# Kernel optimization log

Measured on AMD Instinct MI355X. Metric: run time of the kernel, lower is better.

The kernel has to match this reference:

```python
import jax, jax.numpy as jnp
import numpy as np

LATENT = 256

def setup_inputs() -> dict:
    key = jax.random.key(0)
    k1, k2, k3, k4, k5 = jax.random.split(key, 5)
    B, Te, Td, D = 4, 512, 256, LATENT
    encoder_output = jax.random.normal(k1, (B, Te, D), dtype=jnp.float32)
    decoder_output = jax.random.normal(k2, (B, Td, D), dtype=jnp.float32)
    # 'random_normal' keras initializer: stddev 0.05
    W_a = jax.random.normal(k3, (D, D), dtype=jnp.float32) * 0.05
    U_a = jax.random.normal(k4, (D, D), dtype=jnp.float32) * 0.05
    V_a = jax.random.normal(k5, (D, 1), dtype=jnp.float32) * 0.05
    return {"encoder_output": encoder_output, "decoder_output": decoder_output,
            "W_a": W_a, "U_a": U_a, "V_a": V_a}

def reference(encoder_output, decoder_output, W_a, U_a, V_a):
    # Projections computed once per position (mathematically equal to the
    # tiled tensordots in the original, without redundant GEMM work).
    W_enc = jnp.einsum('bed,df->bef', encoder_output, W_a)   # [B,Te,D]
    U_dec = jnp.einsum('btd,df->btf', decoder_output, U_a)   # [B,Td,D]
    # Broadcast add replaces the explicit tf.tile: [B,Td,Te,D]
    e = jnp.tanh(W_enc[:, None, :, :] + U_dec[:, :, None, :])
    score = jnp.einsum('bted,do->bte', e, V_a[:, 0:1])        # [B,Td,Te]
    attention_weights = jax.nn.softmax(score, axis=-1)
    context_vector = jnp.einsum('bte,bed->btd', attention_weights, encoder_output)
    return (context_vector, attention_weights)
```

## Files before the change

### kernel.cpp

```cpp
#include <hip/hip_runtime.h>

#define B 4
#define TE 512
#define TD 256
#define D 256

#define C2    2.8853900817779268f
#define LOG2E 1.4426950408889634f

__global__ __launch_bounds__(512) void proj_kernel(
    const float* __restrict__ enc, const float* __restrict__ dec,
    const float* __restrict__ Wa,  const float* __restrict__ Ua,
    float* __restrict__ ewt, float* __restrict__ eu)
{
    __shared__ float a_lds[8 * 256];
    const int tid = threadIdx.x;
    const int blk = blockIdx.x;
    const bool is_enc = blk < 256;
    const float* __restrict__ A = is_enc ? enc : dec;
    const float* __restrict__ W = is_enc ? Wa  : Ua;
    const int row0 = (is_enc ? blk : blk - 256) * 8;

    ((float4*)a_lds)[tid] = ((const float4*)(A + (size_t)row0 * 256))[tid];
    __syncthreads();

    const int rh  = tid >> 8;
    const int col = tid & 255;

    float c0 = 0.f, c1 = 0.f, c2 = 0.f, c3 = 0.f;
    const float* __restrict__ ar = &a_lds[rh * 4 * 256];

    #pragma unroll 4
    for (int k = 0; k < 256; k += 4) {
        const float w0 = W[(k + 0) * 256 + col];
        const float w1 = W[(k + 1) * 256 + col];
        const float w2 = W[(k + 2) * 256 + col];
        const float w3 = W[(k + 3) * 256 + col];
        const float4 a0 = *(const float4*)&ar[0 * 256 + k];
        const float4 a1 = *(const float4*)&ar[1 * 256 + k];
        const float4 a2 = *(const float4*)&ar[2 * 256 + k];
        const float4 a3 = *(const float4*)&ar[3 * 256 + k];
        c0 = fmaf(a0.x, w0, c0); c0 = fmaf(a0.y, w1, c0); c0 = fmaf(a0.z, w2, c0); c0 = fmaf(a0.w, w3, c0);
        c1 = fmaf(a1.x, w0, c1); c1 = fmaf(a1.y, w1, c1); c1 = fmaf(a1.z, w2, c1); c1 = fmaf(a1.w, w3, c1);
        c2 = fmaf(a2.x, w0, c2); c2 = fmaf(a2.y, w1, c2); c2 = fmaf(a2.z, w2, c2); c2 = fmaf(a2.w, w3, c2);
        c3 = fmaf(a3.x, w0, c3); c3 = fmaf(a3.y, w1, c3); c3 = fmaf(a3.z, w2, c3); c3 = fmaf(a3.w, w3, c3);
    }

    float4 f;
    f.x = __builtin_amdgcn_exp2f(c0 * C2);
    f.y = __builtin_amdgcn_exp2f(c1 * C2);
    f.z = __builtin_amdgcn_exp2f(c2 * C2);
    f.w = __builtin_amdgcn_exp2f(c3 * C2);

    if (is_enc) {
        const int b  = row0 >> 9;
        const int e0 = (row0 & 511) + rh * 4;
        *(float4*)&ewt[((size_t)(b * 256 + col)) * 512 + e0] = f;
    } else {
        const int r0 = row0 + rh * 4;
        eu[(r0 + 0) * 256 + col] = f.x;
        eu[(r0 + 1) * 256 + col] = f.y;
        eu[(r0 + 2) * 256 + col] = f.z;
        eu[(r0 + 3) * 256 + col] = f.w;
    }
}

__global__ __launch_bounds__(512) void attn_kernel(
    const float* __restrict__ enc, const float* __restrict__ ewt,
    const float* __restrict__ eu,  const float* __restrict__ Va,
    float* __restrict__ ctx, float* __restrict__ aw)
{
    __shared__ float eul[2 * 256];
    __shared__ float val[256];
    __shared__ float sc[2][TE];
    __shared__ float wred[2][2][4];
    __shared__ float part[2][2][256];

    const int tid = threadIdx.x;
    const int b   = blockIdx.x >> 7;
    const int tp  = blockIdx.x & 127;
    const int bt0 = b * 256 + tp * 2;

    if (tid < 256) val[tid] = Va[tid];
    eul[tid] = eu[(size_t)bt0 * 256 + tid];
    __syncthreads();

    {
        const float* __restrict__ ewb = ewt + (size_t)b * 256 * 512 + tid;
        float q0 = 0.f, q1 = 0.f;

        for (int d = 0; d < 256; d += 8) {
            float w[8];
            #pragma unroll
            for (int j = 0; j < 8; j++) w[j] = ewb[(d + j) * 512];

            #pragma unroll
            for (int h = 0; h < 2; h++) {
                const int dd = d + h * 4;
                const float4 v4 = *(const float4*)&val[dd];
                const float4 a0 = *(const float4*)&eul[dd];
                const float4 a1 = *(const float4*)&eul[256 + dd];
                const float* wj = &w[h * 4];

                q0 += v4.x * __builtin_amdgcn_rcpf(fmaf(wj[0], a0.x, 1.0f));
                q0 += v4.y * __builtin_amdgcn_rcpf(fmaf(wj[1], a0.y, 1.0f));
                q0 += v4.z * __builtin_amdgcn_rcpf(fmaf(wj[2], a0.z, 1.0f));
                q0 += v4.w * __builtin_amdgcn_rcpf(fmaf(wj[3], a0.w, 1.0f));

                q1 += v4.x * __builtin_amdgcn_rcpf(fmaf(wj[0], a1.x, 1.0f));
                q1 += v4.y * __builtin_amdgcn_rcpf(fmaf(wj[1], a1.y, 1.0f));
                q1 += v4.z * __builtin_amdgcn_rcpf(fmaf(wj[2], a1.z, 1.0f));
                q1 += v4.w * __builtin_amdgcn_rcpf(fmaf(wj[3], a1.w, 1.0f));
            }
        }
        sc[0][tid] = -2.0f * q0;
        sc[1][tid] = -2.0f * q1;
    }
    __syncthreads();

    {
        const int wv   = tid >> 6;
        const int lane = tid & 63;
        const int t    = wv >> 2;
        const int seg  = wv & 3;
        float* __restrict__ srow = &sc[t][seg * 128];

        const float x0 = srow[lane];
        const float x1 = srow[lane + 64];

        float m = fmaxf(x0, x1);
        #pragma unroll
        for (int s = 32; s > 0; s >>= 1) m = fmaxf(m, __shfl_xor(m, s, 64));
        if (lane == 0) wred[0][t][seg] = m;
        __syncthreads();
        const float4 mm = *(const float4*)&wred[0][t][0];
        const float M = fmaxf(fmaxf(mm.x, mm.y), fmaxf(mm.z, mm.w));

        const float g0 = __builtin_amdgcn_exp2f((x0 - M) * LOG2E);
        const float g1 = __builtin_amdgcn_exp2f((x1 - M) * LOG2E);

        float ssum = g0 + g1;
        #pragma unroll
        for (int s = 32; s > 0; s >>= 1) ssum += __shfl_xor(ssum, s, 64);
        if (lane == 0) wred[1][t][seg] = ssum;
        __syncthreads();
        const float4 sm = *(const float4*)&wred[1][t][0];
        const float inv = __builtin_amdgcn_rcpf((sm.x + sm.y) + (sm.z + sm.w));

        const float p0 = g0 * inv, p1 = g1 * inv;
        srow[lane]      = p0;
        srow[lane + 64] = p1;
        float* __restrict__ ao = aw + ((size_t)(bt0 + t)) * 512 + seg * 128;
        ao[lane]      = p0;
        ao[lane + 64] = p1;
    }
    __syncthreads();

    {
        const int eg = tid >> 8;
        const int dl = tid & 255;
        const float* __restrict__ eb =
            enc + ((size_t)b * 512 + eg * 256) * 256 + dl;
        const int e0 = eg * 256;

        float c0 = 0.f, c1 = 0.f;
        #pragma unroll 2
        for (int j = 0; j < 256; j += 8) {
            float r[8];
            #pragma unroll
            for (int u = 0; u < 8; u++) r[u] = eb[(j + u) * 256];
            #pragma unroll
            for (int h = 0; h < 2; h++) {
                const float4 w0 = *(const float4*)&sc[0][e0 + j + h * 4];
                const float4 w1 = *(const float4*)&sc[1][e0 + j + h * 4];
                const float* ru = &r[h * 4];
                c0 = fmaf(w0.x, ru[0], c0); c0 = fmaf(w0.y, ru[1], c0);
                c0 = fmaf(w0.z, ru[2], c0); c0 = fmaf(w0.w, ru[3], c0);
                c1 = fmaf(w1.x, ru[0], c1); c1 = fmaf(w1.y, ru[1], c1);
                c1 = fmaf(w1.z, ru[2], c1); c1 = fmaf(w1.w, ru[3], c1);
            }
        }
        part[eg][0][dl] = c0;
        part[eg][1][dl] = c1;
    }
    __syncthreads();

    {
        const int t  = tid >> 8;
        const int dl = tid & 255;
        ctx[((size_t)(bt0 + t)) * 256 + dl] = part[0][t][dl] + part[1][t][dl];
    }
}

extern "C" void kernel_launch(void* const* d_in, const int* in_sizes, int n_in,
                              void* d_out, int out_size, void* d_ws, size_t ws_size,
                              hipStream_t stream) {
    const float* enc = (const float*)d_in[0];
    const float* dec = (const float*)d_in[1];
    const float* Wa  = (const float*)d_in[2];
    const float* Ua  = (const float*)d_in[3];
    const float* Va  = (const float*)d_in[4];

    float* out = (float*)d_out;
    float* ctx = out;
    float* aw  = out + B * TD * D;

    float* ewt = (float*)d_ws;
    float* eu  = ewt + (size_t)B * D * TE;

    proj_kernel<<<dim3(384), dim3(512), 0, stream>>>(enc, dec, Wa, Ua, ewt, eu);
    attn_kernel<<<dim3(512), dim3(512), 0, stream>>>(enc, ewt, eu, Va, ctx, aw);
}
```

Before: 113.0 us.

## Combine reciprocals algebraically, widen attention blocks to four rows, retile projection

The score loop now merges four 1/(1+w*a) terms into one fraction, so it issues one reciprocal per four terms instead of four. The attention kernel handles four decoder rows per 1024-thread block instead of two, so each encoder tile load feeds twice as many rows in both the score and context phases. The projection kernel uses 256 threads with eight rows per thread. Risks include overflow or precision loss in the product of four denominators, and fewer blocks (256) on a device with many CUs.

```diff
diff --git a/kernel.cpp b/kernel.cpp
--- a/kernel.cpp
+++ b/kernel.cpp
@@ -8,7 +8,7 @@
 #define C2    2.8853900817779268f
 #define LOG2E 1.4426950408889634f
 
-__global__ __launch_bounds__(512) void proj_kernel(
+__global__ __launch_bounds__(256) void proj_kernel(
     const float* __restrict__ enc, const float* __restrict__ dec,
     const float* __restrict__ Wa,  const float* __restrict__ Ua,
     float* __restrict__ ewt, float* __restrict__ eu)
@@ -21,72 +21,88 @@
     const float* __restrict__ W = is_enc ? Wa  : Ua;
     const int row0 = (is_enc ? blk : blk - 256) * 8;
 
-    ((float4*)a_lds)[tid] = ((const float4*)(A + (size_t)row0 * 256))[tid];
-    __syncthreads();
-
-    const int rh  = tid >> 8;
-    const int col = tid & 255;
-
-    float c0 = 0.f, c1 = 0.f, c2 = 0.f, c3 = 0.f;
-    const float* __restrict__ ar = &a_lds[rh * 4 * 256];
+    {
+        const float4* src = (const float4*)(A + (size_t)row0 * 256);
+        ((float4*)a_lds)[tid]       = src[tid];
+        ((float4*)a_lds)[tid + 256] = src[tid + 256];
+    }
+    __syncthreads();
+
+    float acc[8] = {0.f,0.f,0.f,0.f,0.f,0.f,0.f,0.f};
 
     #pragma unroll 4
     for (int k = 0; k < 256; k += 4) {
-        const float w0 = W[(k + 0) * 256 + col];
-        const float w1 = W[(k + 1) * 256 + col];
-        const float w2 = W[(k + 2) * 256 + col];
-        const float w3 = W[(k + 3) * 256 + col];
-        const float4 a0 = *(const float4*)&ar[0 * 256 + k];
-        const float4 a1 = *(const float4*)&ar[1 * 256 + k];
-        const float4 a2 = *(const float4*)&ar[2 * 256 + k];
-        const float4 a3 = *(const float4*)&ar[3 * 256 + k];
-        c0 = fmaf(a0.x, w0, c0); c0 = fmaf(a0.y, w1, c0); c0 = fmaf(a0.z, w2, c0); c0 = fmaf(a0.w, w3, c0);
-        c1 = fmaf(a1.x, w0, c1); c1 = fmaf(a1.y, w1, c1); c1 = fmaf(a1.z, w2, c1); c1 = fmaf(a1.w, w3, c1);
-        c2 = fmaf(a2.x, w0, c2); c2 = fmaf(a2.y, w1, c2); c2 = fmaf(a2.z, w2, c2); c2 = fmaf(a2.w, w3, c2);
-        c3 = fmaf(a3.x, w0, c3); c3 = fmaf(a3.y, w1, c3); c3 = fmaf(a3.z, w2, c3); c3 = fmaf(a3.w, w3, c3);
-    }
-
-    float4 f;
-    f.x = __builtin_amdgcn_exp2f(c0 * C2);
-    f.y = __builtin_amdgcn_exp2f(c1 * C2);
-    f.z = __builtin_amdgcn_exp2f(c2 * C2);
-    f.w = __builtin_amdgcn_exp2f(c3 * C2);
+        const float w0 = W[(k + 0) * 256 + tid];
+        const float w1 = W[(k + 1) * 256 + tid];
+        const float w2 = W[(k + 2) * 256 + tid];
+        const float w3 = W[(k + 3) * 256 + tid];
+        #pragma unroll
+        for (int r = 0; r < 8; r++) {
+            const float4 a4 = *(const float4*)&a_lds[r * 256 + k];
+            acc[r] = fmaf(a4.x, w0, acc[r]);
+            acc[r] = fmaf(a4.y, w1, acc[r]);
+            acc[r] = fmaf(a4.z, w2, acc[r]);
+            acc[r] = fmaf(a4.w, w3, acc[r]);
+        }
+    }
+
+    float f[8];
+    #pragma unroll
+    for (int r = 0; r < 8; r++)
+        f[r] = __builtin_amdgcn_exp2f(acc[r] * C2);
 
     if (is_enc) {
         const int b  = row0 >> 9;
-        const int e0 = (row0 & 511) + rh * 4;
-        *(float4*)&ewt[((size_t)(b * 256 + col)) * 512 + e0] = f;
+        const int e0 = row0 & 511;
+        float* o = ewt + ((size_t)(b * 256 + tid)) * 512 + e0;
+        *(float4*)(o + 0) = make_float4(f[0], f[1], f[2], f[3]);
+        *(float4*)(o + 4) = make_float4(f[4], f[5], f[6], f[7]);
     } else {
-        const int r0 = row0 + rh * 4;
-        eu[(r0 + 0) * 256 + col] = f.x;
-        eu[(r0 + 1) * 256 + col] = f.y;
-        eu[(r0 + 2) * 256 + col] = f.z;
-        eu[(r0 + 3) * 256 + col] = f.w;
-    }
-}
-
-__global__ __launch_bounds__(512) void attn_kernel(
+        #pragma unroll
+        for (int r = 0; r < 8; r++)
+            eu[(row0 + r) * 256 + tid] = f[r];
+    }
+}
+
+__device__ __forceinline__ void qcomb4(float& q, const float4& v,
+                                       float p0, float p1, float p2, float p3)
+{
+    const float n01 = fmaf(v.y, p0, v.x * p1);
+    const float d01 = p0 * p1;
+    const float n23 = fmaf(v.w, p2, v.z * p3);
+    const float d23 = p2 * p3;
+    const float num = fmaf(n23, d01, n01 * d23);
+    const float den = d01 * d23;
+    q = fmaf(num, __builtin_amdgcn_rcpf(den), q);
+}
+
+__global__ __launch_bounds__(1024) void attn_kernel(
     const float* __restrict__ enc, const float* __restrict__ ewt,
     const float* __restrict__ eu,  const float* __restrict__ Va,
     float* __restrict__ ctx, float* __restrict__ aw)
 {
-    __shared__ float eul[2 * 256];
+    __shared__ float eul[4 * 256];
     __shared__ float val[256];
-    __shared__ float sc[2][TE];
-    __shared__ float wred[2][2][4];
-    __shared__ float part[2][2][256];
+    __shared__ float sc[4][TE];
+    __shared__ float wred[2][4][4];
+    __shared__ float part[4][4][256];
 
     const int tid = threadIdx.x;
-    const int b   = blockIdx.x >> 7;
-    const int tp  = blockIdx.x & 127;
-    const int bt0 = b * 256 + tp * 2;
+    const int b   = blockIdx.x >> 6;
+    const int t0  = (blockIdx.x & 63) * 4;
+    const int bt0 = b * 256 + t0;
 
     if (tid < 256) val[tid] = Va[tid];
     eul[tid] = eu[(size_t)bt0 * 256 + tid];
     __syncthreads();
 
     {
-        const float* __restrict__ ewb = ewt + (size_t)b * 256 * 512 + tid;
+        const int e  = tid & 511;
+        const int tp = tid >> 9;
+        const float* __restrict__ ewb = ewt + (size_t)b * 256 * 512 + e;
+        const float* __restrict__ ea0 = &eul[(2 * tp + 0) * 256];
+        const float* __restrict__ ea1 = &eul[(2 * tp + 1) * 256];
+
         float q0 = 0.f, q1 = 0.f;
 
         for (int d = 0; d < 256; d += 8) {
@@ -98,23 +114,20 @@
             for (int h = 0; h < 2; h++) {
                 const int dd = d + h * 4;
                 const float4 v4 = *(const float4*)&val[dd];
-                const float4 a0 = *(const float4*)&eul[dd];
-                const float4 a1 = *(const float4*)&eul[256 + dd];
+                const float4 a0 = *(const float4*)&ea0[dd];
+                const float4 a1 = *(const float4*)&ea1[dd];
                 const float* wj = &w[h * 4];
 
-                q0 += v4.x * __builtin_amdgcn_rcpf(fmaf(wj[0], a0.x, 1.0f));
-                q0 += v4.y * __builtin_amdgcn_rcpf(fmaf(wj[1], a0.y, 1.0f));
-                q0 += v4.z * __builtin_amdgcn_rcpf(fmaf(wj[2], a0.z, 1.0f));
-                q0 += v4.w * __builtin_amdgcn_rcpf(fmaf(wj[3], a0.w, 1.0f));
-
-                q1 += v4.x * __builtin_amdgcn_rcpf(fmaf(wj[0], a1.x, 1.0f));
-                q1 += v4.y * __builtin_amdgcn_rcpf(fmaf(wj[1], a1.y, 1.0f));
-                q1 += v4.z * __builtin_amdgcn_rcpf(fmaf(wj[2], a1.z, 1.0f));
-                q1 += v4.w * __builtin_amdgcn_rcpf(fmaf(wj[3], a1.w, 1.0f));
+                qcomb4(q0, v4,
+                       fmaf(wj[0], a0.x, 1.0f), fmaf(wj[1], a0.y, 1.0f),
+                       fmaf(wj[2], a0.z, 1.0f), fmaf(wj[3], a0.w, 1.0f));
+                qcomb4(q1, v4,
+                       fmaf(wj[0], a1.x, 1.0f), fmaf(wj[1], a1.y, 1.0f),
+                       fmaf(wj[2], a1.z, 1.0f), fmaf(wj[3], a1.w, 1.0f));
             }
         }
-        sc[0][tid] = -2.0f * q0;
-        sc[1][tid] = -2.0f * q1;
+        sc[2 * tp + 0][e] = -2.0f * q0;
+        sc[2 * tp + 1][e] = -2.0f * q1;
     }
     __syncthreads();
 
@@ -160,35 +173,38 @@
         const int eg = tid >> 8;
         const int dl = tid & 255;
         const float* __restrict__ eb =
-            enc + ((size_t)b * 512 + eg * 256) * 256 + dl;
-        const int e0 = eg * 256;
-
-        float c0 = 0.f, c1 = 0.f;
-        #pragma unroll 2
-        for (int j = 0; j < 256; j += 8) {
-            float r[8];
-            #pragma unroll
-            for (int u = 0; u < 8; u++) r[u] = eb[(j + u) * 256];
-            #pragma unroll
-            for (int h = 0; h < 2; h++) {
-                const float4 w0 = *(const float4*)&sc[0][e0 + j + h * 4];
-                const float4 w1 = *(const float4*)&sc[1][e0 + j + h * 4];
-                const float* ru = &r[h * 4];
-                c0 = fmaf(w0.x, ru[0], c0); c0 = fmaf(w0.y, ru[1], c0);
-                c0 = fmaf(w0.z, ru[2], c0); c0 = fmaf(w0.w, ru[3], c0);
-                c1 = fmaf(w1.x, ru[0], c1); c1 = fmaf(w1.y, ru[1], c1);
-                c1 = fmaf(w1.z, ru[2], c1); c1 = fmaf(w1.w, ru[3], c1);
-            }
+            enc + ((size_t)b * 512 + eg * 128) * 256 + dl;
+        const int e0 = eg * 128;
+
+        float c0 = 0.f, c1 = 0.f, c2 = 0.f, c3 = 0.f;
+        #pragma unroll 4
+        for (int j = 0; j < 128; j += 4) {
+            const float4 w0 = *(const float4*)&sc[0][e0 + j];
+            const float4 w1 = *(const float4*)&sc[1][e0 + j];
+            const float4 w2 = *(const float4*)&sc[2][e0 + j];
+            const float4 w3 = *(const float4*)&sc[3][e0 + j];
+            const float r0 = eb[(j + 0) * 256];
+            const float r1 = eb[(j + 1) * 256];
+            const float r2 = eb[(j + 2) * 256];
+            const float r3 = eb[(j + 3) * 256];
+            c0 = fmaf(w0.x, r0, c0); c0 = fmaf(w0.y, r1, c0); c0 = fmaf(w0.z, r2, c0); c0 = fmaf(w0.w, r3, c0);
+            c1 = fmaf(w1.x, r0, c1); c1 = fmaf(w1.y, r1, c1); c1 = fmaf(w1.z, r2, c1); c1 = fmaf(w1.w, r3, c1);
+            c2 = fmaf(w2.x, r0, c2); c2 = fmaf(w2.y, r1, c2); c2 = fmaf(w2.z, r2, c2); c2 = fmaf(w2.w, r3, c2);
+            c3 = fmaf(w3.x, r0, c3); c3 = fmaf(w3.y, r1, c3); c3 = fmaf(w3.z, r2, c3); c3 = fmaf(w3.w, r3, c3);
         }
         part[eg][0][dl] = c0;
         part[eg][1][dl] = c1;
+        part[eg][2][dl] = c2;
+        part[eg][3][dl] = c3;
     }
     __syncthreads();
 
     {
         const int t  = tid >> 8;
         const int dl = tid & 255;
-        ctx[((size_t)(bt0 + t)) * 256 + dl] = part[0][t][dl] + part[1][t][dl];
+        ctx[((size_t)(bt0 + t)) * 256 + dl] =
+            (part[0][t][dl] + part[1][t][dl]) +
+            (part[2][t][dl] + part[3][t][dl]);
     }
 }
 
@@ -208,6 +224,6 @@
     float* ewt = (float*)d_ws;
     float* eu  = ewt + (size_t)B * D * TE;
 
-    proj_kernel<<<dim3(384), dim3(512), 0, stream>>>(enc, dec, Wa, Ua, ewt, eu);
-    attn_kernel<<<dim3(512), dim3(512), 0, stream>>>(enc, ewt, eu, Va, ctx, aw);
-}
+    proj_kernel<<<dim3(384), dim3(256), 0, stream>>>(enc, dec, Wa, Ua, ewt, eu);
+    attn_kernel<<<dim3(256), dim3(1024), 0, stream>>>(enc, ewt, eu, Va, ctx, aw);
+}
```

New measurement: 106.5 us. 1.06x faster.
